# Kernel optimization log

Measured on AMD Instinct MI355X. Metric: run time of the kernel, lower is better.

Reference implementation:

```python
import jax, jax.numpy as jnp
import numpy as np

K_SIZE = 5  # kernel_size


def _patches(f, k):
    # f: (b, c, h, w) -> (b, c, k*k, h, w), matching torch.nn.Unfold ordering
    # (patch positions row-major (kh, kw) per channel), padding = k//2, stride 1.
    p = k // 2
    b, c, h, w = f.shape
    fp = jnp.pad(f, ((0, 0), (0, 0), (p, p), (p, p)))
    slices = [fp[:, :, i:i + h, j:j + w] for i in range(k) for j in range(k)]
    return jnp.stack(slices, axis=2)


def _conv1x1(w, b, f):
    # w: (out, in), b: (out,), f: (b, in, h, w)
    return jnp.einsum('oc,bchw->bohw', w, f) + b[None, :, None, None]


def setup_inputs() -> dict:
    key = jax.random.key(0)
    ks = jax.random.split(key, 8)
    B, XC, YC, FT, H, W = 4, 64, 64, 64, 128, 128
    x = jax.random.normal(ks[0], (B, XC, H, W), dtype=jnp.float32)
    y = jax.random.normal(ks[1], (B, YC, H, W), dtype=jnp.float32)
    sx = 1.0 / np.sqrt(XC)
    sy = 1.0 / np.sqrt(YC)
    sf = 1.0 / np.sqrt(FT)
    wx = jax.random.uniform(ks[2], (FT, XC), jnp.float32, -sx, sx)
    bx = jax.random.uniform(ks[3], (FT,), jnp.float32, -sx, sx)
    wy = jax.random.uniform(ks[4], (FT, YC), jnp.float32, -sy, sy)
    by = jax.random.uniform(ks[5], (FT,), jnp.float32, -sy, sy)
    wo = jax.random.uniform(ks[6], (XC, FT), jnp.float32, -sf, sf)
    bo = jax.random.uniform(ks[7], (XC,), jnp.float32, -sf, sf)
    return {"x": x, "y": y, "wx": wx, "bx": bx, "wy": wy, "by": by, "wo": wo, "bo": bo}


def reference(x, y, wx, bx, wy, by, wo, bo):
    k = K_SIZE
    q = _conv1x1(wy, by, y)            # (b, feat, h, w): Q (the q axis of size 1 is squeezed)
    Kp = _patches(q, k)                # (b, feat, k^2, h, w): unfold(conv_y(y))
    v = _conv1x1(wx, bx, x)            # (b, feat, h, w)
    Vp = _patches(v, k)                # (b, feat, k^2, h, w): unfold(conv_x(x))
    A = jnp.einsum('bckhw,bchw->bkhw', Kp, q)   # scores over k^2 neighbors
    A = jax.nn.softmax(A, axis=1)               # softmax over dim=1 (k^2)
    out = jnp.einsum('bkhw,bckhw->bchw', A, Vp)  # aggregate values
    out = _conv1x1(wo, bo, out)
    return out + x
```

## Files before the change

kernel.cpp:

```cpp
#include <hip/hip_runtime.h>

#define HH   128
#define WW   128
#define HW   (HH * WW)
#define CC   64
#define TILE 16
#define HALO 20
#define NHP  (HALO * HALO)
#define SWZ(r) (((r) >> 1) & 7)

typedef unsigned int uint32;
typedef _Float16 h2   __attribute__((ext_vector_type(2)));
typedef __fp16   h2b  __attribute__((ext_vector_type(2)));
typedef _Float16 h8   __attribute__((ext_vector_type(8)));
typedef float    f32x4 __attribute__((ext_vector_type(4)));

__device__ __forceinline__ uint32 pkrtz(float a, float b) {
    h2b r = __builtin_amdgcn_cvt_pkrtz(a, b);
    return __builtin_bit_cast(uint32, r);
}
__device__ __forceinline__ float dot2(uint32 a, uint32 b, float c) {
#if __has_builtin(__builtin_amdgcn_fdot2)
    return __builtin_amdgcn_fdot2(__builtin_bit_cast(h2b, a),
                                  __builtin_bit_cast(h2b, b), c, false);
#else
    h2 x = __builtin_bit_cast(h2, a), y = __builtin_bit_cast(h2, b);
    return c + (float)x.x * (float)y.x + (float)x.y * (float)y.y;
#endif
}
__device__ __forceinline__ f32x4 mfma16(uint4 a, uint4 b, f32x4 c) {
    return __builtin_amdgcn_mfma_f32_16x16x32_f16(
        __builtin_bit_cast(h8, a), __builtin_bit_cast(h8, b), c, 0, 0, 0);
}
__device__ __forceinline__ uint4 pack_w8(const float* __restrict__ w) {
    const float4 lo = *(const float4*)w;
    const float4 hi = *(const float4*)(w + 4);
    uint4 r;
    r.x = pkrtz(lo.x, lo.y); r.y = pkrtz(lo.z, lo.w);
    r.z = pkrtz(hi.x, hi.y); r.w = pkrtz(hi.z, hi.w);
    return r;
}

__global__ __attribute__((amdgpu_flat_work_group_size(1024, 1024),
                          amdgpu_waves_per_eu(4, 4)))
void fused_attn(const float* __restrict__ x, const float* __restrict__ y,
                const float* __restrict__ wx, const float* __restrict__ bx,
                const float* __restrict__ wy, const float* __restrict__ by,
                const float* __restrict__ wo, const float* __restrict__ bo,
                float* __restrict__ out)
{
    __shared__ uint32 Ah[NHP * 32];
    __shared__ uint32 Bh[NHP * 32];

    const int lin  = blockIdx.x;
    const int xcd  = lin & 7;
    const int rr   = lin >> 3;
    const int b    = xcd >> 1;
    const int half = xcd & 1;
    const int ty0  = ((rr >> 3) + half * 4) * TILE;
    const int tx0  = (rr & 7) * TILE;

    const int t = threadIdx.x;

    if (t < 800) {
        const int cg  = t / 200;
        const int rem = t - cg * 200;
        const int hy  = rem / 10;
        const int hx  = (rem - hy * 10) * 2;
        const int pix = hy * HALO + hx;
        int gy = ty0 + hy - 2, gx = tx0 + hx - 2;
        const bool ok = ((unsigned)gy < HH) & ((unsigned)gx < (WW - 1));
        if (!ok) { gy = 0; gx = 0; }
        const size_t base = (size_t)b * CC * HW + (size_t)(cg * 16) * HW
                          + (size_t)gy * WW + gx;
        const int w0 = ((cg * 2    ) ^ SWZ(pix)) * 4;
        const int w1 = ((cg * 2 + 1) ^ SWZ(pix)) * 4;
        const int w2 = ((cg * 2    ) ^ SWZ(pix + 1)) * 4;
        const int w3 = ((cg * 2 + 1) ^ SWZ(pix + 1)) * 4;
        {
            float2 v[16];
            #pragma unroll
            for (int j = 0; j < 16; ++j)
                v[j] = *(const float2*)(y + base + (size_t)j * HW);
            uint4 q0, q1, q2, q3;
            q0.x = pkrtz(v[0].x,  v[1].x);  q0.y = pkrtz(v[2].x,  v[3].x);
            q0.z = pkrtz(v[4].x,  v[5].x);  q0.w = pkrtz(v[6].x,  v[7].x);
            q1.x = pkrtz(v[8].x,  v[9].x);  q1.y = pkrtz(v[10].x, v[11].x);
            q1.z = pkrtz(v[12].x, v[13].x); q1.w = pkrtz(v[14].x, v[15].x);
            q2.x = pkrtz(v[0].y,  v[1].y);  q2.y = pkrtz(v[2].y,  v[3].y);
            q2.z = pkrtz(v[4].y,  v[5].y);  q2.w = pkrtz(v[6].y,  v[7].y);
            q3.x = pkrtz(v[8].y,  v[9].y);  q3.y = pkrtz(v[10].y, v[11].y);
            q3.z = pkrtz(v[12].y, v[13].y); q3.w = pkrtz(v[14].y, v[15].y);
            *(uint4*)&Ah[pix * 32 + w0]       = q0;
            *(uint4*)&Ah[pix * 32 + w1]       = q1;
            *(uint4*)&Ah[(pix + 1) * 32 + w2] = q2;
            *(uint4*)&Ah[(pix + 1) * 32 + w3] = q3;
        }
        {
            float2 v[16];
            #pragma unroll
            for (int j = 0; j < 16; ++j)
                v[j] = *(const float2*)(x + base + (size_t)j * HW);
            uint4 q0, q1, q2, q3;
            q0.x = pkrtz(v[0].x,  v[1].x);  q0.y = pkrtz(v[2].x,  v[3].x);
            q0.z = pkrtz(v[4].x,  v[5].x);  q0.w = pkrtz(v[6].x,  v[7].x);
            q1.x = pkrtz(v[8].x,  v[9].x);  q1.y = pkrtz(v[10].x, v[11].x);
            q1.z = pkrtz(v[12].x, v[13].x); q1.w = pkrtz(v[14].x, v[15].x);
            q2.x = pkrtz(v[0].y,  v[1].y);  q2.y = pkrtz(v[2].y,  v[3].y);
            q2.z = pkrtz(v[4].y,  v[5].y);  q2.w = pkrtz(v[6].y,  v[7].y);
            q3.x = pkrtz(v[8].y,  v[9].y);  q3.y = pkrtz(v[10].y, v[11].y);
            q3.z = pkrtz(v[12].y, v[13].y); q3.w = pkrtz(v[14].y, v[15].y);
            *(uint4*)&Bh[pix * 32 + w0]       = q0;
            *(uint4*)&Bh[pix * 32 + w1]       = q1;
            *(uint4*)&Bh[(pix + 1) * 32 + w2] = q2;
            *(uint4*)&Bh[(pix + 1) * 32 + w3] = q3;
        }
    }
    __syncthreads();

    const int wv = t >> 6;
    const int ln = t & 63;
    const int lm = ln & 15;
    const int qd = ln >> 4;
    const int ot = wv & 3;

    f32x4 accq[7], accv[7];
    uint2 xres[4];
    {
        const uint4 aq0 = pack_w8(wy + (ot * 16 + lm) * CC + qd * 8);
        const uint4 aq1 = pack_w8(wy + (ot * 16 + lm) * CC + qd * 8 + 32);
        const uint4 av0 = pack_w8(wx + (ot * 16 + lm) * CC + qd * 8);
        const uint4 av1 = pack_w8(wx + (ot * 16 + lm) * CC + qd * 8 + 32);
        #pragma unroll
        for (int k = 0; k < 7; ++k) {
            const int j = wv + k * 16;
            if (j < 100) {
                const int px = (j >> 2) * 16 + lm, sw = SWZ(px);
                const uint4 b0 = *(const uint4*)&Ah[px * 32 + ((qd    ) ^ sw) * 4];
                const uint4 b1 = *(const uint4*)&Ah[px * 32 + ((qd + 4) ^ sw) * 4];
                f32x4 a = {0.f, 0.f, 0.f, 0.f};
                a = mfma16(aq0, b0, a); a = mfma16(aq1, b1, a); accq[k] = a;
                const uint4 c0 = *(const uint4*)&Bh[px * 32 + ((qd    ) ^ sw) * 4];
                const uint4 c1 = *(const uint4*)&Bh[px * 32 + ((qd + 4) ^ sw) * 4];
                f32x4 v = {0.f, 0.f, 0.f, 0.f};
                v = mfma16(av0, c0, v); v = mfma16(av1, c1, v); accv[k] = v;
            }
        }
        #pragma unroll
        for (int k = 0; k < 4; ++k) {
            const int px = ((wv >> 2) + k * 4) * 16 + lm;
            const int hpix = ((px >> 4) + 2) * HALO + (px & 15) + 2;
            const int chunk = ot * 2 + (qd >> 1);
            xres[k] = *(const uint2*)
                &Bh[hpix * 32 + (chunk ^ SWZ(hpix)) * 4 + (qd & 1) * 2];
        }
    }
    __syncthreads();

    {
        const float4 bq = *(const float4*)(by + ot * 16 + qd * 4);
        const float4 bv = *(const float4*)(bx + ot * 16 + qd * 4);
        const int chunk = ot * 2 + (qd >> 1);
        #pragma unroll
        for (int k = 0; k < 7; ++k) {
            const int j = wv + k * 16;
            if (j < 100) {
                const int px = (j >> 2) * 16 + lm;
                const int hy = px / HALO, hx = px - hy * HALO;
                const int gy = ty0 + hy - 2, gx = tx0 + hx - 2;
                uint2 wq = {0u, 0u}, wvv = {0u, 0u};
                if (((unsigned)gy < HH) & ((unsigned)gx < WW)) {
                    wq.x  = pkrtz(accq[k].x + bq.x, accq[k].y + bq.y);
                    wq.y  = pkrtz(accq[k].z + bq.z, accq[k].w + bq.w);
                    wvv.x = pkrtz(accv[k].x + bv.x, accv[k].y + bv.y);
                    wvv.y = pkrtz(accv[k].z + bv.z, accv[k].w + bv.w);
                }
                const int off = px * 32 + (chunk ^ SWZ(px)) * 4 + (qd & 1) * 2;
                *(uint2*)&Ah[off] = wq;
                *(uint2*)&Bh[off] = wvv;
            }
        }
    }
    __syncthreads();

    const int p    = t >> 2, sub = t & 3;
    const int py   = p >> 4, pxl = p & 15;
    const int crow = (py + 2) * HALO + (pxl + 2);

    uint32 qc[8];
    {
        const int c0 = ((2 * sub)     ^ SWZ(crow)) * 4;
        const int c1 = ((2 * sub + 1) ^ SWZ(crow)) * 4;
        *(uint4*)&qc[0] = *(const uint4*)&Ah[crow * 32 + c0];
        *(uint4*)&qc[4] = *(const uint4*)&Ah[crow * 32 + c1];
    }

    float sc[25];
    #pragma unroll
    for (int dy = 0; dy < 5; ++dy)
        #pragma unroll
        for (int dx = 0; dx < 5; ++dx) {
            const int nrow = (py + dy) * HALO + (pxl + dx);
            const int c0 = ((2 * sub)     ^ SWZ(nrow)) * 4;
            const int c1 = ((2 * sub + 1) ^ SWZ(nrow)) * 4;
            const uint4 r0 = *(const uint4*)&Ah[nrow * 32 + c0];
            const uint4 r1 = *(const uint4*)&Ah[nrow * 32 + c1];
            float s = 0.f;
            s = dot2(qc[0], r0.x, s); s = dot2(qc[1], r0.y, s);
            s = dot2(qc[2], r0.z, s); s = dot2(qc[3], r0.w, s);
            s = dot2(qc[4], r1.x, s); s = dot2(qc[5], r1.y, s);
            s = dot2(qc[6], r1.z, s); s = dot2(qc[7], r1.w, s);
            s += __shfl_xor(s, 1);
            s += __shfl_xor(s, 2);
            sc[dy * 5 + dx] = s;
        }

    float mx = sc[24];
    #pragma unroll
    for (int k = 0; k < 24; k += 2) mx = fmaxf(mx, fmaxf(sc[k], sc[k + 1]));
    #pragma unroll
    for (int k = 0; k < 25; ++k) sc[k] = __expf(sc[k] - mx);
    float sum = sc[24];
    #pragma unroll
    for (int k = 0; k < 24; k += 2) sum += sc[k] + sc[k + 1];
    const float inv = 1.f / sum;

    h2 ag[8];
    #pragma unroll
    for (int k = 0; k < 8; ++k) ag[k] = (h2)(_Float16)0;
    #pragma unroll
    for (int dy = 0; dy < 5; ++dy)
        #pragma unroll
        for (int dx = 0; dx < 5; ++dx) {
            const int nrow = (py + dy) * HALO + (pxl + dx);
            const int c0 = ((2 * sub)     ^ SWZ(nrow)) * 4;
            const int c1 = ((2 * sub + 1) ^ SWZ(nrow)) * 4;
            const uint4 r0 = *(const uint4*)&Bh[nrow * 32 + c0];
            const uint4 r1 = *(const uint4*)&Bh[nrow * 32 + c1];
            const _Float16 af = (_Float16)(sc[dy * 5 + dx] * inv);
            const h2 a2 = {af, af};
            ag[0] += a2 * __builtin_bit_cast(h2, r0.x);
            ag[1] += a2 * __builtin_bit_cast(h2, r0.y);
            ag[2] += a2 * __builtin_bit_cast(h2, r0.z);
            ag[3] += a2 * __builtin_bit_cast(h2, r0.w);
            ag[4] += a2 * __builtin_bit_cast(h2, r1.x);
            ag[5] += a2 * __builtin_bit_cast(h2, r1.y);
            ag[6] += a2 * __builtin_bit_cast(h2, r1.z);
            ag[7] += a2 * __builtin_bit_cast(h2, r1.w);
        }

    __syncthreads();

    {
        const int c0 = ((2 * sub)     ^ SWZ(p)) * 4;
        const int c1 = ((2 * sub + 1) ^ SWZ(p)) * 4;
        uint4 w0, w1;
        w0.x = __builtin_bit_cast(uint32, ag[0]); w0.y = __builtin_bit_cast(uint32, ag[1]);
        w0.z = __builtin_bit_cast(uint32, ag[2]); w0.w = __builtin_bit_cast(uint32, ag[3]);
        w1.x = __builtin_bit_cast(uint32, ag[4]); w1.y = __builtin_bit_cast(uint32, ag[5]);
        w1.z = __builtin_bit_cast(uint32, ag[6]); w1.w = __builtin_bit_cast(uint32, ag[7]);
        *(uint4*)&Ah[p * 32 + c0] = w0;
        *(uint4*)&Ah[p * 32 + c1] = w1;
    }
    __syncthreads();

    {
        const uint4 a0 = pack_w8(wo + (ot * 16 + lm) * CC + qd * 8);
        const uint4 a1 = pack_w8(wo + (ot * 16 + lm) * CC + qd * 8 + 32);
        const float4 bq = *(const float4*)(bo + ot * 16 + qd * 4);
        #pragma unroll
        for (int k = 0; k < 4; ++k) {
            const int px = ((wv >> 2) + k * 4) * 16 + lm, sw = SWZ(px);
            const uint4 b0 = *(const uint4*)&Ah[px * 32 + ((qd    ) ^ sw) * 4];
            const uint4 b1 = *(const uint4*)&Ah[px * 32 + ((qd + 4) ^ sw) * 4];
            f32x4 a = {0.f, 0.f, 0.f, 0.f};
            a = mfma16(a0, b0, a);
            a = mfma16(a1, b1, a);
            const int gh = ty0 + (px >> 4), gw = tx0 + (px & 15);
            const h2 xp0 = __builtin_bit_cast(h2, xres[k].x);
            const h2 xp1 = __builtin_bit_cast(h2, xres[k].y);
            const float rv[4] = {(float)xp0.x, (float)xp0.y,
                                 (float)xp1.x, (float)xp1.y};
            const float av4[4] = {a.x + bq.x, a.y + bq.y, a.z + bq.z, a.w + bq.w};
            #pragma unroll
            for (int r = 0; r < 4; ++r) {
                const int oc = ot * 16 + qd * 4 + r;
                const size_t ad = (size_t)(b * CC + oc) * HW + (size_t)gh * WW + gw;
                out[ad] = av4[r] + rv[r];
            }
        }
    }
}

extern "C" void kernel_launch(void* const* d_in, const int* in_sizes, int n_in,
                              void* d_out, int out_size, void* d_ws, size_t ws_size,
                              hipStream_t stream) {
    const float* x  = (const float*)d_in[0];
    const float* y  = (const float*)d_in[1];
    const float* wx = (const float*)d_in[2];
    const float* bx = (const float*)d_in[3];
    const float* wy = (const float*)d_in[4];
    const float* by = (const float*)d_in[5];
    const float* wo = (const float*)d_in[6];
    const float* bo = (const float*)d_in[7];
    float* out = (float*)d_out;
    (void)d_ws; (void)ws_size;

    fused_attn<<<dim3(256), 1024, 0, stream>>>(x, y, wx, bx, wy, by, wo, bo, out);
}
```

Before: 114.8 us.

## Split Q and V projections to overlap x loads with Q MFMA

Issues the global loads for both y and x up front, but stages only y into shared memory before the first barrier. That barrier waits only on LDS counters, so the x loads can stay in flight while the Q projection MFMAs run. The x tile is then packed into shared memory, and the V projection moves into a later phase, with barriers rearranged so the Q and V writebacks and the score and aggregation phases stay correctly ordered. This hides global load latency behind compute, at the cost of holding 32 extra registers for the x values across the Q phase, which could lower occupancy.

After: 115.6 us. About the same (+0.7%).

```diff
diff --git a/kernel.cpp b/kernel.cpp
--- a/kernel.cpp
+++ b/kernel.cpp
@@ -61,8 +61,11 @@
     const int tx0  = (rr & 7) * TILE;
 
     const int t = threadIdx.x;
-
-    if (t < 800) {
+    const bool doStage = t < 800;
+
+    float2 xv[16];
+    int pixS = 0, cgS = 0;
+    if (doStage) {
         const int cg  = t / 200;
         const int rem = t - cg * 200;
         const int hy  = rem / 10;
@@ -73,50 +76,31 @@
         if (!ok) { gy = 0; gx = 0; }
         const size_t base = (size_t)b * CC * HW + (size_t)(cg * 16) * HW
                           + (size_t)gy * WW + gx;
-        const int w0 = ((cg * 2    ) ^ SWZ(pix)) * 4;
-        const int w1 = ((cg * 2 + 1) ^ SWZ(pix)) * 4;
-        const int w2 = ((cg * 2    ) ^ SWZ(pix + 1)) * 4;
-        const int w3 = ((cg * 2 + 1) ^ SWZ(pix + 1)) * 4;
-        {
-            float2 v[16];
-            #pragma unroll
-            for (int j = 0; j < 16; ++j)
-                v[j] = *(const float2*)(y + base + (size_t)j * HW);
-            uint4 q0, q1, q2, q3;
-            q0.x = pkrtz(v[0].x,  v[1].x);  q0.y = pkrtz(v[2].x,  v[3].x);
-            q0.z = pkrtz(v[4].x,  v[5].x);  q0.w = pkrtz(v[6].x,  v[7].x);
-            q1.x = pkrtz(v[8].x,  v[9].x);  q1.y = pkrtz(v[10].x, v[11].x);
-            q1.z = pkrtz(v[12].x, v[13].x); q1.w = pkrtz(v[14].x, v[15].x);
-            q2.x = pkrtz(v[0].y,  v[1].y);  q2.y = pkrtz(v[2].y,  v[3].y);
-            q2.z = pkrtz(v[4].y,  v[5].y);  q2.w = pkrtz(v[6].y,  v[7].y);
-            q3.x = pkrtz(v[8].y,  v[9].y);  q3.y = pkrtz(v[10].y, v[11].y);
-            q3.z = pkrtz(v[12].y, v[13].y); q3.w = pkrtz(v[14].y, v[15].y);
-            *(uint4*)&Ah[pix * 32 + w0]       = q0;
-            *(uint4*)&Ah[pix * 32 + w1]       = q1;
-            *(uint4*)&Ah[(pix + 1) * 32 + w2] = q2;
-            *(uint4*)&Ah[(pix + 1) * 32 + w3] = q3;
-        }
-        {
-            float2 v[16];
-            #pragma unroll
-            for (int j = 0; j < 16; ++j)
-                v[j] = *(const float2*)(x + base + (size_t)j * HW);
-            uint4 q0, q1, q2, q3;
-            q0.x = pkrtz(v[0].x,  v[1].x);  q0.y = pkrtz(v[2].x,  v[3].x);
-            q0.z = pkrtz(v[4].x,  v[5].x);  q0.w = pkrtz(v[6].x,  v[7].x);
-            q1.x = pkrtz(v[8].x,  v[9].x);  q1.y = pkrtz(v[10].x, v[11].x);
-            q1.z = pkrtz(v[12].x, v[13].x); q1.w = pkrtz(v[14].x, v[15].x);
-            q2.x = pkrtz(v[0].y,  v[1].y);  q2.y = pkrtz(v[2].y,  v[3].y);
-            q2.z = pkrtz(v[4].y,  v[5].y);  q2.w = pkrtz(v[6].y,  v[7].y);
-            q3.x = pkrtz(v[8].y,  v[9].y);  q3.y = pkrtz(v[10].y, v[11].y);
-            q3.z = pkrtz(v[12].y, v[13].y); q3.w = pkrtz(v[14].y, v[15].y);
-            *(uint4*)&Bh[pix * 32 + w0]       = q0;
-            *(uint4*)&Bh[pix * 32 + w1]       = q1;
-            *(uint4*)&Bh[(pix + 1) * 32 + w2] = q2;
-            *(uint4*)&Bh[(pix + 1) * 32 + w3] = q3;
-        }
-    }
-    __syncthreads();
+        pixS = pix; cgS = cg;
+        float2 yv[16];
+        #pragma unroll
+        for (int j = 0; j < 16; ++j)
+            yv[j] = *(const float2*)(y + base + (size_t)j * HW);
+        #pragma unroll
+        for (int j = 0; j < 16; ++j)
+            xv[j] = *(const float2*)(x + base + (size_t)j * HW);
+        uint4 q0, q1, q2, q3;
+        q0.x = pkrtz(yv[0].x,  yv[1].x);  q0.y = pkrtz(yv[2].x,  yv[3].x);
+        q0.z = pkrtz(yv[4].x,  yv[5].x);  q0.w = pkrtz(yv[6].x,  yv[7].x);
+        q1.x = pkrtz(yv[8].x,  yv[9].x);  q1.y = pkrtz(yv[10].x, yv[11].x);
+        q1.z = pkrtz(yv[12].x, yv[13].x); q1.w = pkrtz(yv[14].x, yv[15].x);
+        q2.x = pkrtz(yv[0].y,  yv[1].y);  q2.y = pkrtz(yv[2].y,  yv[3].y);
+        q2.z = pkrtz(yv[4].y,  yv[5].y);  q2.w = pkrtz(yv[6].y,  yv[7].y);
+        q3.x = pkrtz(yv[8].y,  yv[9].y);  q3.y = pkrtz(yv[10].y, yv[11].y);
+        q3.z = pkrtz(yv[12].y, yv[13].y); q3.w = pkrtz(yv[14].y, yv[15].y);
+        *(uint4*)&Ah[pix * 32 + ((cg * 2    ) ^ SWZ(pix)) * 4]         = q0;
+        *(uint4*)&Ah[pix * 32 + ((cg * 2 + 1) ^ SWZ(pix)) * 4]         = q1;
+        *(uint4*)&Ah[(pix + 1) * 32 + ((cg * 2    ) ^ SWZ(pix + 1)) * 4] = q2;
+        *(uint4*)&Ah[(pix + 1) * 32 + ((cg * 2 + 1) ^ SWZ(pix + 1)) * 4] = q3;
+    }
+    asm volatile("s_waitcnt lgkmcnt(0)" ::: "memory");
+    __builtin_amdgcn_s_barrier();
+    asm volatile("" ::: "memory");
 
     const int wv = t >> 6;
     const int ln = t & 63;
@@ -124,13 +108,10 @@
     const int qd = ln >> 4;
     const int ot = wv & 3;
 
-    f32x4 accq[7], accv[7];
-    uint2 xres[4];
+    f32x4 accq[7];
     {
         const uint4 aq0 = pack_w8(wy + (ot * 16 + lm) * CC + qd * 8);
         const uint4 aq1 = pack_w8(wy + (ot * 16 + lm) * CC + qd * 8 + 32);
-        const uint4 av0 = pack_w8(wx + (ot * 16 + lm) * CC + qd * 8);
-        const uint4 av1 = pack_w8(wx + (ot * 16 + lm) * CC + qd * 8 + 32);
         #pragma unroll
         for (int k = 0; k < 7; ++k) {
             const int j = wv + k * 16;
@@ -139,27 +120,32 @@
                 const uint4 b0 = *(const uint4*)&Ah[px * 32 + ((qd    ) ^ sw) * 4];
                 const uint4 b1 = *(const uint4*)&Ah[px * 32 + ((qd + 4) ^ sw) * 4];
                 f32x4 a = {0.f, 0.f, 0.f, 0.f};
-                a = mfma16(aq0, b0, a); a = mfma16(aq1, b1, a); accq[k] = a;
-                const uint4 c0 = *(const uint4*)&Bh[px * 32 + ((qd    ) ^ sw) * 4];
-                const uint4 c1 = *(const uint4*)&Bh[px * 32 + ((qd + 4) ^ sw) * 4];
-                f32x4 v = {0.f, 0.f, 0.f, 0.f};
-                v = mfma16(av0, c0, v); v = mfma16(av1, c1, v); accv[k] = v;
-            }
-        }
-        #pragma unroll
-        for (int k = 0; k < 4; ++k) {
-            const int px = ((wv >> 2) + k * 4) * 16 + lm;
-            const int hpix = ((px >> 4) + 2) * HALO + (px & 15) + 2;
-            const int chunk = ot * 2 + (qd >> 1);
-            xres[k] = *(const uint2*)
-                &Bh[hpix * 32 + (chunk ^ SWZ(hpix)) * 4 + (qd & 1) * 2];
-        }
+                a = mfma16(aq0, b0, a); a = mfma16(aq1, b1, a);
+                accq[k] = a;
+            }
+        }
+    }
+    if (doStage) {
+        uint4 q0, q1, q2, q3;
+        q0.x = pkrtz(xv[0].x,  xv[1].x);  q0.y = pkrtz(xv[2].x,  xv[3].x);
+        q0.z = pkrtz(xv[4].x,  xv[5].x);  q0.w = pkrtz(xv[6].x,  xv[7].x);
+        q1.x = pkrtz(xv[8].x,  xv[9].x);  q1.y = pkrtz(xv[10].x, xv[11].x);
+        q1.z = pkrtz(xv[12].x, xv[13].x); q1.w = pkrtz(xv[14].x, xv[15].x);
+        q2.x = pkrtz(xv[0].y,  xv[1].y);  q2.y = pkrtz(xv[2].y,  xv[3].y);
+        q2.z = pkrtz(xv[4].y,  xv[5].y);  q2.w = pkrtz(xv[6].y,  xv[7].y);
+        q3.x = pkrtz(xv[8].y,  xv[9].y);  q3.y = pkrtz(xv[10].y, xv[11].y);
+        q3.z = pkrtz(xv[12].y, xv[13].y); q3.w = pkrtz(xv[14].y, xv[15].y);
+        *(uint4*)&Bh[pixS * 32 + ((cgS * 2    ) ^ SWZ(pixS)) * 4]         = q0;
+        *(uint4*)&Bh[pixS * 32 + ((cgS * 2 + 1) ^ SWZ(pixS)) * 4]         = q1;
+        *(uint4*)&Bh[(pixS + 1) * 32 + ((cgS * 2    ) ^ SWZ(pixS + 1)) * 4] = q2;
+        *(uint4*)&Bh[(pixS + 1) * 32 + ((cgS * 2 + 1) ^ SWZ(pixS + 1)) * 4] = q3;
     }
     __syncthreads();
 
+    f32x4 accv[7];
+    uint2 xres[4];
     {
         const float4 bq = *(const float4*)(by + ot * 16 + qd * 4);
-        const float4 bv = *(const float4*)(bx + ot * 16 + qd * 4);
         const int chunk = ot * 2 + (qd >> 1);
         #pragma unroll
         for (int k = 0; k < 7; ++k) {
@@ -168,21 +154,57 @@
                 const int px = (j >> 2) * 16 + lm;
                 const int hy = px / HALO, hx = px - hy * HALO;
                 const int gy = ty0 + hy - 2, gx = tx0 + hx - 2;
-                uint2 wq = {0u, 0u}, wvv = {0u, 0u};
+                uint2 wq = {0u, 0u};
                 if (((unsigned)gy < HH) & ((unsigned)gx < WW)) {
-                    wq.x  = pkrtz(accq[k].x + bq.x, accq[k].y + bq.y);
-                    wq.y  = pkrtz(accq[k].z + bq.z, accq[k].w + bq.w);
+                    wq.x = pkrtz(accq[k].x + bq.x, accq[k].y + bq.y);
+                    wq.y = pkrtz(accq[k].z + bq.z, accq[k].w + bq.w);
+                }
+                *(uint2*)&Ah[px * 32 + (chunk ^ SWZ(px)) * 4 + (qd & 1) * 2] = wq;
+            }
+        }
+        const uint4 av0 = pack_w8(wx + (ot * 16 + lm) * CC + qd * 8);
+        const uint4 av1 = pack_w8(wx + (ot * 16 + lm) * CC + qd * 8 + 32);
+        #pragma unroll
+        for (int k = 0; k < 7; ++k) {
+            const int j = wv + k * 16;
+            if (j < 100) {
+                const int px = (j >> 2) * 16 + lm, sw = SWZ(px);
+                const uint4 c0 = *(const uint4*)&Bh[px * 32 + ((qd    ) ^ sw) * 4];
+                const uint4 c1 = *(const uint4*)&Bh[px * 32 + ((qd + 4) ^ sw) * 4];
+                f32x4 v = {0.f, 0.f, 0.f, 0.f};
+                v = mfma16(av0, c0, v); v = mfma16(av1, c1, v);
+                accv[k] = v;
+            }
+        }
+        #pragma unroll
+        for (int k = 0; k < 4; ++k) {
+            const int px = ((wv >> 2) + k * 4) * 16 + lm;
+            const int hpix = ((px >> 4) + 2) * HALO + (px & 15) + 2;
+            xres[k] = *(const uint2*)
+                &Bh[hpix * 32 + (chunk ^ SWZ(hpix)) * 4 + (qd & 1) * 2];
+        }
+    }
+    __syncthreads();
+
+    {
+        const float4 bv = *(const float4*)(bx + ot * 16 + qd * 4);
+        const int chunk = ot * 2 + (qd >> 1);
+        #pragma unroll
+        for (int k = 0; k < 7; ++k) {
+            const int j = wv + k * 16;
+            if (j < 100) {
+                const int px = (j >> 2) * 16 + lm;
+                const int hy = px / HALO, hx = px - hy * HALO;
+                const int gy = ty0 + hy - 2, gx = tx0 + hx - 2;
+                uint2 wvv = {0u, 0u};
+                if (((unsigned)gy < HH) & ((unsigned)gx < WW)) {
                     wvv.x = pkrtz(accv[k].x + bv.x, accv[k].y + bv.y);
                     wvv.y = pkrtz(accv[k].z + bv.z, accv[k].w + bv.w);
                 }
-                const int off = px * 32 + (chunk ^ SWZ(px)) * 4 + (qd & 1) * 2;
-                *(uint2*)&Ah[off] = wq;
-                *(uint2*)&Bh[off] = wvv;
-            }
-        }
-    }
-    __syncthreads();
-
+                *(uint2*)&Bh[px * 32 + (chunk ^ SWZ(px)) * 4 + (qd & 1) * 2] = wvv;
+            }
+        }
+    }
     const int p    = t >> 2, sub = t & 3;
     const int py   = p >> 4, pxl = p & 15;
     const int crow = (py + 2) * HALO + (pxl + 2);
@@ -224,6 +246,8 @@
     #pragma unroll
     for (int k = 0; k < 24; k += 2) sum += sc[k] + sc[k + 1];
     const float inv = 1.f / sum;
+
+    __syncthreads();
 
     h2 ag[8];
     #pragma unroll
@@ -248,9 +272,6 @@
             ag[6] += a2 * __builtin_bit_cast(h2, r1.z);
             ag[7] += a2 * __builtin_bit_cast(h2, r1.w);
         }
-
-    __syncthreads();
-
     {
         const int c0 = ((2 * sub)     ^ SWZ(p)) * 4;
         const int c1 = ((2 * sub + 1) ^ SWZ(p)) * 4;
```
